# Optimization experiments

Hardware: AMD Instinct MI355X
Metric: run time of the kernel (lower is better)

The kernel has to match this reference:

```python
import jax, jax.numpy as jnp
import numpy as np

B, T, HID = 1, 2048, 2048
H, KVH, D = 32, 8, 64
G = H // KVH          # kv groups = 4
SCALE = 1.0 / np.sqrt(D)
NEG = -1e9


def _rotate_half(x):
    x1, x2 = x[..., : D // 2], x[..., D // 2 :]
    return jnp.concatenate((-x2, x1), axis=-1)


def setup_inputs() -> dict:
    key = jax.random.key(0)
    ks = jax.random.split(key, 8)
    hidden_states = jax.random.normal(ks[0], (B, T, HID), jnp.float32)
    # RoPE tables (faithful shapes; realistic values)
    pos = jnp.arange(T, dtype=jnp.float32)[:, None]
    inv = 1.0 / (10000.0 ** (jnp.arange(0, D, 2, dtype=jnp.float32) / D))
    ang = pos * inv[None, :]                      # [T, D/2]
    ang = jnp.concatenate([ang, ang], axis=-1)    # [T, D]
    cos = jnp.broadcast_to(jnp.cos(ang)[None], (B, T, D))
    sin = jnp.broadcast_to(jnp.sin(ang)[None], (B, T, D))
    # causal additive mask [B,1,T,T]
    causal = jnp.tril(jnp.ones((T, T), bool))
    attention_mask_4d = jnp.where(causal, 0.0, NEG).astype(jnp.float32)[None, None]
    s = 0.02
    Wq = jax.random.normal(ks[1], (H * D, HID), jnp.float32) * s
    Wk = jax.random.normal(ks[2], (KVH * D, HID), jnp.float32) * s
    Wv = jax.random.normal(ks[3], (KVH * D, HID), jnp.float32) * s
    Wo = jax.random.normal(ks[4], (HID, H * D), jnp.float32) * s
    return {"hidden_states": hidden_states, "cos": cos, "sin": sin,
            "attention_mask_4d": attention_mask_4d,
            "Wq": Wq, "Wk": Wk, "Wv": Wv, "Wo": Wo}


def reference(hidden_states, cos, sin, attention_mask_4d, Wq, Wk, Wv, Wo):
    x = hidden_states
    b, t, _ = x.shape
    # QKV projections (nn.Linear: x @ W.T), then [B, heads, T, D]
    q = (x @ Wq.T).reshape(b, t, H, D).transpose(0, 2, 1, 3)
    k = (x @ Wk.T).reshape(b, t, KVH, D).transpose(0, 2, 1, 3)
    v = (x @ Wv.T).reshape(b, t, KVH, D).transpose(0, 2, 1, 3)
    # rotary: cos/sin [B,T,D] -> broadcast over heads
    c = cos[:, None]; s = sin[:, None]
    q = q * c + _rotate_half(q) * s
    k = k * c + _rotate_half(k) * s
    # grouped-query attention with fp32 scores/softmax
    qg = q.reshape(b, KVH, G, t, D)
    scores = jnp.einsum('bkgtd,bksd->bkgts', qg.astype(jnp.float32),
                        k.astype(jnp.float32)) * SCALE
    m = attention_mask_4d[:, 0].astype(jnp.float32)  # [B,T,S]
    scores = scores + m[:, None, None, :, :]
    probs = jax.nn.softmax(scores, axis=-1)
    out = jnp.einsum('bkgts,bksd->bkgtd', probs.astype(v.dtype), v)
    out = out.astype(q.dtype).reshape(b, H, t, D)
    out = out.transpose(0, 2, 1, 3).reshape(b, t, H * D)
    return out @ Wo.T
```

## Files before the change

### kernel.cpp

```cpp
#include <hip/hip_runtime.h>
#include <math.h>

typedef __attribute__((ext_vector_type(8))) __bf16 bf16x8;
typedef __attribute__((ext_vector_type(4))) float  f32x4;
typedef unsigned short ushort_t;
typedef unsigned int   uint_t;

static __device__ inline f32x4 mfma16(bf16x8 a, bf16x8 b, f32x4 c) {
    return __builtin_amdgcn_mfma_f32_16x16x32_bf16(a, b, c, 0, 0, 0);
}

static __device__ inline ushort_t f2b(float f) {
    uint_t u = __builtin_bit_cast(uint_t, f);
    u = (u + 0x7FFFu + ((u >> 16) & 1u)) >> 16;
    return (ushort_t)u;
}
static __device__ inline float b2f(ushort_t u) {
    uint_t x = ((uint_t)u) << 16;
    return __builtin_bit_cast(float, x);
}
static __device__ inline bf16x8 ld8(const ushort_t* p) {
    uint4 v = *(const uint4*)p;
    return __builtin_bit_cast(bf16x8, v);
}
static __device__ inline float fexp2(float x) {
#if __has_builtin(__builtin_amdgcn_exp2f)
    return __builtin_amdgcn_exp2f(x);
#else
    return exp2f(x);
#endif
}

static __device__ inline void gl_lds16(const ushort_t* g, ushort_t* l) {
    __builtin_amdgcn_global_load_lds(
        (const __attribute__((address_space(1))) void*)(g),
        (__attribute__((address_space(3))) void*)(l),
        16, 0, 0);
}

#define WS_XB     0
#define WS_WQKV   8388608
#define WS_WO     20971520
#define WS_P0     29360128
#define WS_P1     41943040
#define WS_QBB    0
#define WS_KBB    8388608
#define WS_VTG    10485760
#define WS_AB     12582912
#define WS_O0     29360128
#define WS_O1     46137344

__global__ __launch_bounds__(256) void cvt_all(const float* __restrict__ x,
                                               const float* __restrict__ wq,
                                               const float* __restrict__ wk,
                                               const float* __restrict__ wv,
                                               const float* __restrict__ wo,
                                               ushort_t* __restrict__ dst) {
    const size_t i = (size_t)(blockIdx.x * 256 + threadIdx.x) * 4;
    const float* src; size_t off;
    if (i < 4194304)       { src = x;  off = 0; }
    else if (i < 8388608)  { src = wq; off = 4194304; }
    else if (i < 9437184)  { src = wk; off = 8388608; }
    else if (i < 10485760) { src = wv; off = 9437184; }
    else                   { src = wo; off = 10485760; }
    float4 v = *(const float4*)(src + (i - off));
    ushort4 o;
    o.x = f2b(v.x); o.y = f2b(v.y); o.z = f2b(v.z); o.w = f2b(v.w);
    *(ushort4*)(dst + i) = o;
}

template <int OUTB>
__global__ __launch_bounds__(512, 2) void gemm256(const ushort_t* __restrict__ A,
                                                  const ushort_t* __restrict__ Bt,
                                                  void* __restrict__ C0,
                                                  void* __restrict__ C1,
                                                  int N, int K) {
    __shared__ ushort_t lds[65536];
    const int tid  = threadIdx.x;
    const int lane = tid & 63, w = tid >> 6;
    const int qn = lane & 15, quad = lane >> 4;
    const long m0 = (long)blockIdx.y * 256;
    const long n0 = (long)blockIdx.x * 256;
    const int kh   = K >> 1;
    const int kbeg = blockIdx.z * kh;
    const int NT   = kh >> 6;
    void* Cout = blockIdx.z ? C1 : C0;
    ushort_t* ldsp = lds;

    const int srow = w * 8 + (lane >> 3);
    const int scol = ((lane & 7) ^ (lane >> 3)) * 8;
    const ushort_t* gA = A  + (m0 + srow) * (size_t)K + kbeg + scol;
    const ushort_t* gB = Bt + (n0 + srow) * (size_t)K + kbeg + scol;

    const int aRow = ((w >> 2) * 64 + qn) * 64;
    const int bRow = ((w & 3) * 32 + qn) * 64;
    const int sw0 = ((quad * 16)      ^ ((qn & 7) << 4)) >> 1;
    const int sw1 = ((64 + quad * 16) ^ ((qn & 7) << 4)) >> 1;

#define STG_A(t, h, buf)                                                       \
    do { if ((t) < NT) {                                                       \
        const ushort_t* g = gA + (size_t)(h) * 128 * K + (t) * 64;             \
        ushort_t* d = ldsp + (buf) * 32768 + (h) * 8192 + w * 512;             \
        gl_lds16(g, d);                                                        \
        gl_lds16(g + 64 * (size_t)K, d + 4096);                                \
    } } while (0)
#define STG_B(t, h, buf)                                                       \
    do { if ((t) < NT) {                                                       \
        const ushort_t* g = gB + (size_t)(h) * 128 * K + (t) * 64;             \
        ushort_t* d = ldsp + (buf) * 32768 + 16384 + (h) * 8192 + w * 512;     \
        gl_lds16(g, d);                                                        \
        gl_lds16(g + 64 * (size_t)K, d + 4096);                                \
    } } while (0)

#define PHASE(cb, p, qr, qc, STAGE, BOUND)                                     \
    do {                                                                       \
        const ushort_t* bA = ldsp + (cb) * 32768 + (qr) * 8192;                \
        const ushort_t* bB = ldsp + (cb) * 32768 + 16384 + (qc) * 8192;        \
        bf16x8 af[4][2], bv[2][2];                                             \
        _Pragma("unroll")                                                      \
        for (int mi = 0; mi < 4; mi++) {                                       \
            af[mi][0] = *(const bf16x8*)(bA + aRow + mi * 1024 + sw0);         \
            af[mi][1] = *(const bf16x8*)(bA + aRow + mi * 1024 + sw1);         \
        }                                                                      \
        _Pragma("unroll")                                                      \
        for (int nj = 0; nj < 2; nj++) {                                       \
            bv[nj][0] = *(const bf16x8*)(bB + bRow + nj * 1024 + sw0);         \
            bv[nj][1] = *(const bf16x8*)(bB + bRow + nj * 1024 + sw1);         \
        }                                                                      \
        asm volatile("" ::: "memory");          \
        STAGE;                                                                 \
        BOUND;                                                                 \
        __builtin_amdgcn_s_barrier();                                          \
        asm volatile("s_waitcnt lgkmcnt(0)" ::: "memory");                     \
        __builtin_amdgcn_sched_barrier(0);                                     \
        __builtin_amdgcn_s_setprio(1);                                         \
        _Pragma("unroll")                                                      \
        for (int mi = 0; mi < 4; mi++)                                         \
            _Pragma("unroll")                                                  \
            for (int nj = 0; nj < 2; nj++) {                                   \
                acc[p][mi][nj] = mfma16(af[mi][0], bv[nj][0], acc[p][mi][nj]); \
                acc[p][mi][nj] = mfma16(af[mi][1], bv[nj][1], acc[p][mi][nj]); \
            }                                                                  \
        __builtin_amdgcn_s_setprio(0);                                         \
        __builtin_amdgcn_s_barrier();                                          \
    } while (0)

    f32x4 acc[4][4][2];
    f32x4 zero = {0.f, 0.f, 0.f, 0.f};
    #pragma unroll
    for (int p = 0; p < 4; p++)
        #pragma unroll
        for (int mi = 0; mi < 4; mi++)
            #pragma unroll
            for (int nj = 0; nj < 2; nj++) acc[p][mi][nj] = zero;

    STG_A(0, 0, 0); STG_B(0, 0, 0); STG_B(0, 1, 0); STG_A(0, 1, 0);
    STG_A(1, 0, 1); STG_B(1, 0, 1);
    asm volatile("s_waitcnt vmcnt(0)" ::: "memory");
    __builtin_amdgcn_s_barrier();

    for (int t2 = 0; t2 < NT; t2 += 2) {
        PHASE(0, 0, 0, 0, STG_B(t2 + 1, 1, 1), (void)0);
        PHASE(0, 1, 0, 1, STG_A(t2 + 1, 1, 1), (void)0);
        PHASE(0, 2, 1, 0, STG_A(t2 + 2, 0, 0), (void)0);
        PHASE(0, 3, 1, 1, STG_B(t2 + 2, 0, 0),
              if (t2 == NT - 2) { asm volatile("s_waitcnt vmcnt(0)" ::: "memory"); }
              else              { asm volatile("s_waitcnt vmcnt(4)" ::: "memory"); });
        PHASE(1, 0, 0, 0, STG_B(t2 + 2, 1, 0), (void)0);
        PHASE(1, 1, 0, 1, STG_A(t2 + 2, 1, 0), (void)0);
        PHASE(1, 2, 1, 0, STG_A(t2 + 3, 0, 1), (void)0);
        PHASE(1, 3, 1, 1, STG_B(t2 + 3, 0, 1),
              asm volatile("s_waitcnt vmcnt(4)" ::: "memory"););
    }
#undef PHASE
#undef STG_A
#undef STG_B

    #pragma unroll
    for (int p = 0; p < 4; p++) {
        const int qr = p >> 1, qc = p & 1;
        #pragma unroll
        for (int mi = 0; mi < 4; mi++)
            #pragma unroll
            for (int nj = 0; nj < 2; nj++) {
                const long row0 = m0 + qr * 128 + (w >> 2) * 64 + mi * 16 + quad * 4;
                const long col  = n0 + qc * 128 + (w & 3) * 32 + nj * 16 + qn;
                #pragma unroll
                for (int r = 0; r < 4; r++) {
                    if (OUTB)
                        ((ushort_t*)Cout)[(row0 + r) * N + col] = f2b(acc[p][mi][nj][r]);
                    else
                        ((float*)Cout)[(row0 + r) * N + col] = acc[p][mi][nj][r];
                }
            }
    }
}

__global__ __launch_bounds__(256) void fuse_crv(const ushort_t* __restrict__ p0,
                                                const ushort_t* __restrict__ p1,
                                                const float* __restrict__ cs,
                                                const float* __restrict__ sn,
                                                ushort_t* __restrict__ qd,
                                                ushort_t* __restrict__ kd,
                                                ushort_t* __restrict__ vt) {
    __shared__ ushort_t tl[64][65];
    const int cx = blockIdx.x;
    const int ty = blockIdx.y;
    const int r  = threadIdx.x >> 2;
    const int c0 = (threadIdx.x & 3) << 4;
    const int t  = ty * 64 + r;
    const size_t base = (size_t)t * 3072 + cx * 64;

    if (cx < 40) {
        const int cp = c0 ^ 32;
        float own[16], par[16];
        #pragma unroll
        for (int jj = 0; jj < 2; jj++) {
            uint4 a = *(const uint4*)(p0 + base + c0 + jj * 8);
            uint4 b = *(const uint4*)(p1 + base + c0 + jj * 8);
            uint4 c = *(const uint4*)(p0 + base + cp + jj * 8);
            uint4 d = *(const uint4*)(p1 + base + cp + jj * 8);
            const ushort_t* pa = (const ushort_t*)&a;
            const ushort_t* pb = (const ushort_t*)&b;
            const ushort_t* pc = (const ushort_t*)&c;
            const ushort_t* pd = (const ushort_t*)&d;
            #pragma unroll
            for (int e = 0; e < 8; e++) {
                own[jj * 8 + e] = b2f(pa[e]) + b2f(pb[e]);
                par[jj * 8 + e] = b2f(pc[e]) + b2f(pd[e]);
            }
        }
        float cs16[16], sn16[16];
        #pragma unroll
        for (int jj = 0; jj < 4; jj++) {
            float4 c4 = *(const float4*)(cs + (size_t)t * 64 + c0 + jj * 4);
            float4 s4 = *(const float4*)(sn + (size_t)t * 64 + c0 + jj * 4);
            cs16[jj * 4 + 0] = c4.x; cs16[jj * 4 + 1] = c4.y;
            cs16[jj * 4 + 2] = c4.z; cs16[jj * 4 + 3] = c4.w;
            sn16[jj * 4 + 0] = s4.x; sn16[jj * 4 + 1] = s4.y;
            sn16[jj * 4 + 2] = s4.z; sn16[jj * 4 + 3] = s4.w;
        }
        const float scale = (cx < 32) ? 0.18033688f : 1.0f;
        union { ushort_t u[16]; uint4 v[2]; } o;
        #pragma unroll
        for (int j = 0; j < 16; j++) {
            const int d = c0 + j;
            const float pr = (d < 32) ? -par[j] : par[j];
            o.u[j] = f2b((own[j] * cs16[j] + pr * sn16[j]) * scale);
        }
        if (cx < 32) {
            ushort_t* dst = qd + (size_t)t * 2048 + cx * 64 + c0;
            *(uint4*)dst = o.v[0]; *(uint4*)(dst + 8) = o.v[1];
        } else {
            ushort_t* dst = kd + (size_t)t * 512 + (cx - 32) * 64 + c0;
            *(uint4*)dst = o.v[0]; *(uint4*)(dst + 8) = o.v[1];
        }
    } else {
        #pragma unroll
        for (int jj = 0; jj < 2; jj++) {
            uint4 a = *(const uint4*)(p0 + base + c0 + jj * 8);
            uint4 b = *(const uint4*)(p1 + base + c0 + jj * 8);
            const ushort_t* pa = (const ushort_t*)&a;
            const ushort_t* pb = (const ushort_t*)&b;
            #pragma unroll
            for (int e = 0; e < 8; e++)
                tl[r][c0 + jj * 8 + e] = f2b(b2f(pa[e]) + b2f(pb[e]));
        }
        __syncthreads();
        const int rr  = threadIdx.x >> 3;
        const int cc8 = (threadIdx.x & 7) * 8;
        const int db = (cx - 40) * 64, tb = ty * 64;
        #pragma unroll
        for (int h = 0; h < 2; h++) {
            const int d = rr + h * 32;
            ushort4 o0, o1;
            o0.x = tl[cc8 + 0][d]; o0.y = tl[cc8 + 1][d];
            o0.z = tl[cc8 + 2][d]; o0.w = tl[cc8 + 3][d];
            o1.x = tl[cc8 + 4][d]; o1.y = tl[cc8 + 5][d];
            o1.z = tl[cc8 + 6][d]; o1.w = tl[cc8 + 7][d];
            *(ushort4*)(vt + (size_t)(db + d) * 2048 + tb + cc8)     = o0;
            *(ushort4*)(vt + (size_t)(db + d) * 2048 + tb + cc8 + 4) = o1;
        }
    }
}

__global__ __launch_bounds__(256) void combine_o(const float4* __restrict__ s0,
                                                 const float4* __restrict__ s1,
                                                 float4* __restrict__ out) {
    for (int i = blockIdx.x * 256 + threadIdx.x; i < 1048576; i += 2048 * 256) {
        float4 a = s0[i], b = s1[i];
        float4 r; r.x = a.x + b.x; r.y = a.y + b.y; r.z = a.z + b.z; r.w = a.w + b.w;
        out[i] = r;
    }
}

__global__ __launch_bounds__(256) void attn_kernel(const ushort_t* __restrict__ Q,
                                                   const ushort_t* __restrict__ Kb,
                                                   const ushort_t* __restrict__ Vt,
                                                   ushort_t* __restrict__ Ob) {
    __shared__ ushort_t Ks[2 * 4096];
    __shared__ ushort_t Vs[2 * 4096];
    __shared__ ushort_t pl[4 * 16 * 80];
    const int tid  = threadIdx.x;
    const int lane = tid & 63, wid = tid >> 6;
    const int qn = lane & 15, quad = lane >> 4;
    const int h   = blockIdx.x & 31;
    const int qb  = 31 - (blockIdx.x >> 5);
    const int kvb = (h >> 2) * 64;
    const int trow = qb * 64 + wid * 16;
    ushort_t* plw = pl + wid * 16 * 80;
    f32x4 zero = {0.f, 0.f, 0.f, 0.f};

    const ushort_t* qpA = Q + (size_t)(trow + qn) * 2048 + h * 64 + quad * 8;
    const bf16x8 qA0 = ld8(qpA), qA1 = ld8(qpA + 32);

    f32x4 oA[4] = {zero, zero, zero, zero};
    float lA[4] = {0.f, 0.f, 0.f, 0.f};
    const int ntiles = qb + 1;

#define STAGE(s0, buf)                                                         \
    do {                                                                       \
        const ushort_t* kg = Kb + (size_t)((s0) + lane) * 512 + kvb + wid * 8; \
        gl_lds16(kg,      Ks + (buf) * 4096 + wid * 512);                      \
        gl_lds16(kg + 32, Ks + (buf) * 4096 + (wid + 4) * 512);                \
        const ushort_t* vg = Vt + (size_t)(kvb + lane) * 2048 + (s0) + wid * 8;\
        gl_lds16(vg,      Vs + (buf) * 4096 + wid * 512);                      \
        gl_lds16(vg + 32, Vs + (buf) * 4096 + (wid + 4) * 512);                \
    } while (0)

#define COMPUTE(s0, buf)                                                       \
    do {                                                                       \
        f32x4 scA[4];                                                          \
        __builtin_amdgcn_s_setprio(1);                                         \
        _Pragma("unroll")                                                      \
        for (int cb = 0; cb < 4; cb++) {                                       \
            const bf16x8 kf0 = *(const bf16x8*)(Ks + (buf) * 4096 + quad * 512 + (cb * 16 + qn) * 8);       \
            const bf16x8 kf1 = *(const bf16x8*)(Ks + (buf) * 4096 + (quad + 4) * 512 + (cb * 16 + qn) * 8); \
            f32x4 s = mfma16(qA0, kf0, zero); scA[cb] = mfma16(qA1, kf1, s);   \
        }                                                                      \
        __builtin_amdgcn_s_setprio(0);                                         \
        const bool needmask = ((s0) + 63 > trow);                              \
        _Pragma("unroll")                                                      \
        for (int i = 0; i < 4; i++) {                                          \
            const int tA = trow + quad * 4 + i;                                \
            _Pragma("unroll")                                                  \
            for (int cb = 0; cb < 4; cb++) {                                   \
                const int col = (s0) + cb * 16 + qn;                           \
                float vA = scA[cb][i];                                         \
                if (needmask) {                                                \
                    if (col > tA) vA = -INFINITY;                              \
                }                                                              \
                const float pA = fexp2(vA);                                    \
                lA[i] += pA;                                                   \
                plw[(quad * 4 + i) * 80 + cb * 16 + qn] = f2b(pA);             \
            }                                                                  \
        }                                                                      \
        const bf16x8 pfA0 = *(const bf16x8*)(plw + qn * 80 + quad * 8);        \
        const bf16x8 pfA1 = *(const bf16x8*)(plw + qn * 80 + 32 + quad * 8);   \
        __builtin_amdgcn_s_setprio(1);                                         \
        _Pragma("unroll")                                                      \
        for (int dcb = 0; dcb < 4; dcb++) {                                    \
            const bf16x8 vf0 = *(const bf16x8*)(Vs + (buf) * 4096 + quad * 512 + (dcb * 16 + qn) * 8);       \
            const bf16x8 vf1 = *(const bf16x8*)(Vs + (buf) * 4096 + (quad + 4) * 512 + (dcb * 16 + qn) * 8); \
            oA[dcb] = mfma16(pfA0, vf0, oA[dcb]);                              \
            oA[dcb] = mfma16(pfA1, vf1, oA[dcb]);                              \
        }                                                                      \
        __builtin_amdgcn_s_setprio(0);                                         \
    } while (0)

    STAGE(0, 0);
    int t = 0;
    for (; t + 2 <= ntiles; t += 2) {
        __syncthreads();
        STAGE((t + 1) * 64, 1);
        COMPUTE(t * 64, 0);
        __syncthreads();
        if (t + 2 < ntiles) STAGE((t + 2) * 64, 0);
        COMPUTE((t + 1) * 64, 1);
    }
    if (t < ntiles) {
        __syncthreads();
        COMPUTE(t * 64, 0);
    }
#undef STAGE
#undef COMPUTE

    #pragma unroll
    for (int i = 0; i < 4; i++) {
        float sA = lA[i];
        #pragma unroll
        for (int off = 1; off < 16; off <<= 1)
            sA += __shfl_xor(sA, off, 64);
        const float invA = 1.0f / sA;
        ushort_t* obA = Ob + (size_t)(trow + quad * 4 + i) * 2048 + h * 64 + qn;
        obA[0]  = f2b(oA[0][i] * invA);
        obA[16] = f2b(oA[1][i] * invA);
        obA[32] = f2b(oA[2][i] * invA);
        obA[48] = f2b(oA[3][i] * invA);
    }
}

extern "C" void kernel_launch(void* const* d_in, const int* in_sizes, int n_in,
                              void* d_out, int out_size, void* d_ws, size_t ws_size,
                              hipStream_t stream) {
    const float* x    = (const float*)d_in[0];
    const float* cosp = (const float*)d_in[1];
    const float* sinp = (const float*)d_in[2];
    const float* Wq = (const float*)d_in[4];
    const float* Wk = (const float*)d_in[5];
    const float* Wv = (const float*)d_in[6];
    const float* Wo = (const float*)d_in[7];
    char* ws = (char*)d_ws;
    (void)ws_size; (void)in_sizes; (void)n_in; (void)out_size;

    ushort_t* xb    = (ushort_t*)(ws + WS_XB);
    ushort_t* wqkvb = (ushort_t*)(ws + WS_WQKV);
    ushort_t* wob   = (ushort_t*)(ws + WS_WO);
    ushort_t* p0    = (ushort_t*)(ws + WS_P0);
    ushort_t* p1    = (ushort_t*)(ws + WS_P1);
    ushort_t* qbb   = (ushort_t*)(ws + WS_QBB);
    ushort_t* kbb   = (ushort_t*)(ws + WS_KBB);
    ushort_t* vtg   = (ushort_t*)(ws + WS_VTG);
    ushort_t* ab    = (ushort_t*)(ws + WS_AB);
    float*    o0    = (float*)   (ws + WS_O0);
    float*    o1    = (float*)   (ws + WS_O1);

    cvt_all<<<14336, 256, 0, stream>>>(x, Wq, Wk, Wv, Wo, xb);

    gemm256<1><<<dim3(12, 8, 2), 512, 0, stream>>>(xb, wqkvb, p0, p1, 3072, 2048);

    fuse_crv<<<dim3(48, 32), 256, 0, stream>>>(p0, p1, cosp, sinp, qbb, kbb, vtg);

    attn_kernel<<<1024, 256, 0, stream>>>(qbb, kbb, vtg, ab);

    gemm256<0><<<dim3(8, 8, 2), 512, 0, stream>>>(ab, wob, o0, o1, 2048, 2048);

    combine_o<<<2048, 256, 0, stream>>>((const float4*)o0, (const float4*)o1,
                                        (float4*)d_out);
}
```

Baseline: 260.2 us.

## Add 256x128-tile pipelined output-projection GEMM and tweak bf16 conversion and LDS padding

Replaces the output projection's 256x256-tile GEMM with a new 256x128-tile kernel that launches twice as many blocks and targets two blocks per CU. It uses swizzled LDS, a double-buffered stage/compute schedule interleaved over four quadrants, and hand-placed waitcnt and barrier instructions. The aim is better CU occupancy and overlap of loads with MFMA on a GEMM whose grid was previously small. The change also swaps the manual float-to-bf16 rounding for the compiler's native conversion and shrinks the attention P-tile LDS row stride from 80 to 68. The 68 stride may change bank-conflict behaviour, and the 16-byte row reads at that stride need 8-byte alignment to hold.

```diff
diff --git a/kernel.cpp b/kernel.cpp
--- a/kernel.cpp
+++ b/kernel.cpp
@@ -11,9 +11,7 @@
 }
 
 static __device__ inline ushort_t f2b(float f) {
-    uint_t u = __builtin_bit_cast(uint_t, f);
-    u = (u + 0x7FFFu + ((u >> 16) & 1u)) >> 16;
-    return (ushort_t)u;
+    return __builtin_bit_cast(ushort_t, (__bf16)f);
 }
 static __device__ inline float b2f(ushort_t u) {
     uint_t x = ((uint_t)u) << 16;
@@ -196,6 +194,130 @@
     }
 }
 
+__global__ __launch_bounds__(512, 2) void gemm_op(const ushort_t* __restrict__ A,
+                                                  const ushort_t* __restrict__ Bt,
+                                                  float* __restrict__ C0,
+                                                  float* __restrict__ C1,
+                                                  int N, int K) {
+    __shared__ ushort_t lds[49152];
+    const int tid  = threadIdx.x;
+    const int lane = tid & 63, w = tid >> 6;
+    const int qn = lane & 15, quad = lane >> 4;
+    const long m0 = (long)blockIdx.y * 256;
+    const long n0 = (long)blockIdx.x * 128;
+    const int kh   = K >> 1;
+    const int kbeg = blockIdx.z * kh;
+    const int NT   = kh >> 6;
+    float* Cout = blockIdx.z ? C1 : C0;
+    ushort_t* ldsp = lds;
+
+    const int srow = w * 8 + (lane >> 3);
+    const int scol = ((lane & 7) ^ (lane >> 3)) * 8;
+    const ushort_t* gA = A + (m0 + srow) * (size_t)K + kbeg + scol;
+    const int srB  = tid >> 3;
+    const int scB  = ((tid & 7) ^ (srB & 7)) * 8;
+    const ushort_t* gB = Bt + (n0 + srB) * (size_t)K + kbeg + scB;
+
+    const int wm = w >> 1, wn = w & 1;
+    const int aRow = (wm * 32 + qn) * 64;
+    const int bRow = (wn * 32 + qn) * 64;
+    const int sw0 = ((quad * 16)      ^ ((qn & 7) << 4)) >> 1;
+    const int sw1 = ((64 + quad * 16) ^ ((qn & 7) << 4)) >> 1;
+
+#define OSTG_A(t, h, buf)                                                      \
+    do { if ((t) < NT) {                                                       \
+        const ushort_t* g = gA + (size_t)(h) * 128 * K + (t) * 64;             \
+        ushort_t* d = ldsp + (buf) * 24576 + (h) * 8192 + w * 512;             \
+        gl_lds16(g, d);                                                        \
+        gl_lds16(g + 64 * (size_t)K, d + 4096);                                \
+    } } while (0)
+#define OSTG_B(t, h, buf)                                                      \
+    do { if ((t) < NT) {                                                       \
+        const ushort_t* g = gB + (size_t)(h) * 64 * K + (t) * 64;              \
+        ushort_t* d = ldsp + (buf) * 24576 + 16384 + (h) * 4096 + w * 512;     \
+        gl_lds16(g, d);                                                        \
+    } } while (0)
+
+#define OPHASE(cb, p, qr, qc, STAGE, BOUND)                                    \
+    do {                                                                       \
+        const ushort_t* bA = ldsp + (cb) * 24576 + (qr) * 8192;                \
+        const ushort_t* bB = ldsp + (cb) * 24576 + 16384 + (qc) * 4096;        \
+        bf16x8 af[2][2], bv[2][2];                                             \
+        _Pragma("unroll")                                                      \
+        for (int mi = 0; mi < 2; mi++) {                                       \
+            af[mi][0] = *(const bf16x8*)(bA + aRow + mi * 1024 + sw0);         \
+            af[mi][1] = *(const bf16x8*)(bA + aRow + mi * 1024 + sw1);         \
+        }                                                                      \
+        _Pragma("unroll")                                                      \
+        for (int nj = 0; nj < 2; nj++) {                                       \
+            bv[nj][0] = *(const bf16x8*)(bB + bRow + nj * 1024 + sw0);         \
+            bv[nj][1] = *(const bf16x8*)(bB + bRow + nj * 1024 + sw1);         \
+        }                                                                      \
+        asm volatile("" ::: "memory");                                         \
+        STAGE;                                                                 \
+        BOUND;                                                                 \
+        __builtin_amdgcn_s_barrier();                                          \
+        asm volatile("s_waitcnt lgkmcnt(0)" ::: "memory");                     \
+        __builtin_amdgcn_sched_barrier(0);                                     \
+        __builtin_amdgcn_s_setprio(1);                                         \
+        _Pragma("unroll")                                                      \
+        for (int mi = 0; mi < 2; mi++)                                         \
+            _Pragma("unroll")                                                  \
+            for (int nj = 0; nj < 2; nj++) {                                   \
+                acc[p][mi][nj] = mfma16(af[mi][0], bv[nj][0], acc[p][mi][nj]); \
+                acc[p][mi][nj] = mfma16(af[mi][1], bv[nj][1], acc[p][mi][nj]); \
+            }                                                                  \
+        __builtin_amdgcn_s_setprio(0);                                         \
+        __builtin_amdgcn_s_barrier();                                          \
+    } while (0)
+
+    f32x4 acc[4][2][2];
+    f32x4 zero = {0.f, 0.f, 0.f, 0.f};
+    #pragma unroll
+    for (int p = 0; p < 4; p++)
+        #pragma unroll
+        for (int mi = 0; mi < 2; mi++)
+            #pragma unroll
+            for (int nj = 0; nj < 2; nj++) acc[p][mi][nj] = zero;
+
+    OSTG_A(0, 0, 0); OSTG_B(0, 0, 0); OSTG_B(0, 1, 0); OSTG_A(0, 1, 0);
+    OSTG_A(1, 0, 1); OSTG_B(1, 0, 1);
+    asm volatile("s_waitcnt vmcnt(0)" ::: "memory");
+    __builtin_amdgcn_s_barrier();
+
+    for (int t2 = 0; t2 < NT; t2 += 2) {
+        OPHASE(0, 0, 0, 0, OSTG_B(t2 + 1, 1, 1), (void)0);
+        OPHASE(0, 1, 0, 1, OSTG_A(t2 + 1, 1, 1), (void)0);
+        OPHASE(0, 2, 1, 0, OSTG_A(t2 + 2, 0, 0), (void)0);
+        OPHASE(0, 3, 1, 1, OSTG_B(t2 + 2, 0, 0),
+               if (t2 == NT - 2) { asm volatile("s_waitcnt vmcnt(0)" ::: "memory"); }
+               else              { asm volatile("s_waitcnt vmcnt(3)" ::: "memory"); });
+        OPHASE(1, 0, 0, 0, OSTG_B(t2 + 2, 1, 0), (void)0);
+        OPHASE(1, 1, 0, 1, OSTG_A(t2 + 2, 1, 0), (void)0);
+        OPHASE(1, 2, 1, 0, OSTG_A(t2 + 3, 0, 1), (void)0);
+        OPHASE(1, 3, 1, 1, OSTG_B(t2 + 3, 0, 1),
+               asm volatile("s_waitcnt vmcnt(3)" ::: "memory"););
+    }
+#undef OPHASE
+#undef OSTG_A
+#undef OSTG_B
+
+    #pragma unroll
+    for (int p = 0; p < 4; p++) {
+        const int qr = p >> 1, qc = p & 1;
+        #pragma unroll
+        for (int mi = 0; mi < 2; mi++)
+            #pragma unroll
+            for (int nj = 0; nj < 2; nj++) {
+                const long row0 = m0 + qr * 128 + wm * 32 + mi * 16 + quad * 4;
+                const long col  = n0 + qc * 64 + wn * 32 + nj * 16 + qn;
+                #pragma unroll
+                for (int r = 0; r < 4; r++)
+                    Cout[(row0 + r) * N + col] = acc[p][mi][nj][r];
+            }
+    }
+}
+
 __global__ __launch_bounds__(256) void fuse_crv(const ushort_t* __restrict__ p0,
                                                 const ushort_t* __restrict__ p1,
                                                 const float* __restrict__ cs,
@@ -300,7 +422,7 @@
                                                    ushort_t* __restrict__ Ob) {
     __shared__ ushort_t Ks[2 * 4096];
     __shared__ ushort_t Vs[2 * 4096];
-    __shared__ ushort_t pl[4 * 16 * 80];
+    __shared__ ushort_t pl[4 * 16 * 68];
     const int tid  = threadIdx.x;
     const int lane = tid & 63, wid = tid >> 6;
     const int qn = lane & 15, quad = lane >> 4;
@@ -308,7 +430,7 @@
     const int qb  = 31 - (blockIdx.x >> 5);
     const int kvb = (h >> 2) * 64;
     const int trow = qb * 64 + wid * 16;
-    ushort_t* plw = pl + wid * 16 * 80;
+    ushort_t* plw = pl + wid * 16 * 68;
     f32x4 zero = {0.f, 0.f, 0.f, 0.f};
 
     const ushort_t* qpA = Q + (size_t)(trow + qn) * 2048 + h * 64 + quad * 8;
@@ -352,11 +474,11 @@
                 }                                                              \
                 const float pA = fexp2(vA);                                    \
                 lA[i] += pA;                                                   \
-                plw[(quad * 4 + i) * 80 + cb * 16 + qn] = f2b(pA);             \
+                plw[(quad * 4 + i) * 68 + cb * 16 + qn] = f2b(pA);             \
             }                                                                  \
         }                                                                      \
-        const bf16x8 pfA0 = *(const bf16x8*)(plw + qn * 80 + quad * 8);        \
-        const bf16x8 pfA1 = *(const bf16x8*)(plw + qn * 80 + 32 + quad * 8);   \
+        const bf16x8 pfA0 = *(const bf16x8*)(plw + qn * 68 + quad * 8);        \
+        const bf16x8 pfA1 = *(const bf16x8*)(plw + qn * 68 + 32 + quad * 8);   \
         __builtin_amdgcn_s_setprio(1);                                         \
         _Pragma("unroll")                                                      \
         for (int dcb = 0; dcb < 4; dcb++) {                                    \
@@ -433,7 +555,7 @@
 
     attn_kernel<<<1024, 256, 0, stream>>>(qbb, kbb, vtg, ab);
 
-    gemm256<0><<<dim3(8, 8, 2), 512, 0, stream>>>(ab, wob, o0, o1, 2048, 2048);
+    gemm_op<<<dim3(16, 8, 2), 512, 0, stream>>>(ab, wob, o0, o1, 2048, 2048);
 
     combine_o<<<2048, 256, 0, stream>>>((const float4*)o0, (const float4*)o1,
                                         (float4*)d_out);
```

Measured after the change: 254.6 us. 2.1% less time.
